# Optimization experiments

Measured on AMD Instinct MI355X. Metric: run time of the kernel, lower is better.

Reference implementation:

```python
import jax, jax.numpy as jnp
import numpy as np

TOP_K = 2


def setup_inputs() -> dict:
    key = jax.random.key(0)
    ks = jax.random.split(key, 5)
    B, S, D, F, E = 2, 1024, 2048, 4096, 8
    scale_in = 1.0 / np.sqrt(D)
    scale_f = 1.0 / np.sqrt(F)
    return {
        "hidden_states": jax.random.normal(ks[0], (B, S, D), dtype=jnp.float32),
        "gate_w": jax.random.normal(ks[1], (D, E), dtype=jnp.float32) * scale_in,
        "w1": jax.random.normal(ks[2], (E, D, F), dtype=jnp.float32) * scale_in,
        "w3": jax.random.normal(ks[3], (E, D, F), dtype=jnp.float32) * scale_in,
        "w2": jax.random.normal(ks[4], (E, F, D), dtype=jnp.float32) * scale_f,
    }


def reference(hidden_states, gate_w, w1, w3, w2):
    orig_shape = hidden_states.shape
    D = orig_shape[-1]
    x = hidden_states.reshape(-1, D)                      # [T, D]
    E = gate_w.shape[-1]

    # Router: replicated linear (no bias), logits in fp32.
    router_logits = (x @ gate_w).astype(jnp.float32)      # [T, E]
    probs = jax.nn.softmax(router_logits, axis=-1)        # [T, E]
    topk_vals, topk_idx = jax.lax.top_k(probs, TOP_K)     # [T, K]
    # renormalize=False: use raw softmax probs of the selected experts.
    # Scatter top-k weights back to a dense [T, E] combine matrix.
    onehot = jax.nn.one_hot(topk_idx, E, dtype=probs.dtype)        # [T, K, E]
    combine = jnp.einsum("tke,tk->te", onehot, topk_vals)          # [T, E]

    # Dense-over-experts SwiGLU (reference for the fused grouped-GEMM).
    gate = jax.nn.silu(jnp.einsum("td,edf->etf", x, w1))  # [E, T, F]
    up = jnp.einsum("td,edf->etf", x, w3)                 # [E, T, F]
    expert_out = jnp.einsum("etf,efd->etd", gate * up, w2)  # [E, T, D]

    # Combine (this is the TP all-reduce + weighted sum in vllm).
    y = jnp.einsum("te,etd->td", combine, expert_out)     # [T, D]
    return y.reshape(orig_shape)
```

## Files before the change

kernel.cpp:

```cpp
#include <hip/hip_runtime.h>

typedef short v8s __attribute__((ext_vector_type(8)));
typedef float v4f __attribute__((ext_vector_type(4)));

#define T_TOK 2048
#define DD 2048
#define FF 4096
#define EE 8
#define BM 128
#define BN 128
#define BK 64
#define MT_MAX 40
#define MAXROWS 5120

#define WS_COUNTS 0
#define WS_FILL   32
#define WS_ROWOFF 64
#define WS_TOPE   128
#define WS_TOPW   (WS_TOPE + T_TOK * 2 * 4)
#define WS_IDS    (WS_TOPW + T_TOK * 2 * 4)
#define WS_WTS    (WS_IDS + MAXROWS * 4)
#define WS_ZERO   (WS_WTS + MAXROWS * 4)
#define WS_H      73984ul

#define SWZ(r, kb) ((r) * 128 + ((kb) ^ ((((r) ^ ((r) >> 3)) & 7) << 4)))

static __device__ __forceinline__ short f2bf(float f) {
  return __builtin_bit_cast(short, static_cast<__bf16>(f));
}

__global__ __launch_bounds__(256) void router_k(
    const float* __restrict__ x, const float* __restrict__ gw,
    int* __restrict__ counts, int* __restrict__ tope, float* __restrict__ topw) {
  const int lane = threadIdx.x & 63;
  const int t = blockIdx.x * 4 + (threadIdx.x >> 6);
  if (t >= T_TOK) return;
  float acc[EE] = {0.f, 0.f, 0.f, 0.f, 0.f, 0.f, 0.f, 0.f};
  const float* xr = x + (size_t)t * DD;
  for (int i = 0; i < DD / 64; ++i) {
    int k = i * 64 + lane;
    float xv = xr[k];
    const v4f* g = (const v4f*)(gw + (size_t)k * EE);
    v4f g0 = g[0], g1 = g[1];
    acc[0] += xv * g0[0]; acc[1] += xv * g0[1]; acc[2] += xv * g0[2]; acc[3] += xv * g0[3];
    acc[4] += xv * g1[0]; acc[5] += xv * g1[1]; acc[6] += xv * g1[2]; acc[7] += xv * g1[3];
  }
  #pragma unroll
  for (int e = 0; e < EE; ++e) {
    #pragma unroll
    for (int off = 32; off > 0; off >>= 1) acc[e] += __shfl_xor(acc[e], off);
  }
  if (lane == 0) {
    float m = acc[0];
    #pragma unroll
    for (int e = 1; e < EE; ++e) m = fmaxf(m, acc[e]);
    float p[EE], s = 0.f;
    #pragma unroll
    for (int e = 0; e < EE; ++e) { p[e] = expf(acc[e] - m); s += p[e]; }
    float inv = 1.f / s;
    #pragma unroll
    for (int e = 0; e < EE; ++e) p[e] *= inv;
    int e1 = 0;
    #pragma unroll
    for (int e = 1; e < EE; ++e) if (p[e] > p[e1]) e1 = e;
    int e2 = (e1 == 0) ? 1 : 0;
    #pragma unroll
    for (int e = 0; e < EE; ++e) if (e != e1 && p[e] > p[e2]) e2 = e;
    tope[2 * t] = e1;  tope[2 * t + 1] = e2;
    topw[2 * t] = p[e1]; topw[2 * t + 1] = p[e2];
    atomicAdd(&counts[e1], 1);
    atomicAdd(&counts[e2], 1);
  }
}

__global__ void offsets_k(const int* __restrict__ counts, int* __restrict__ rowoff) {
  if (threadIdx.x == 0) {
    int off = 0;
    #pragma unroll
    for (int e = 0; e < EE; ++e) {
      rowoff[e] = off;
      off += ((counts[e] + BM - 1) / BM) * BM;
    }
  }
}

__global__ __launch_bounds__(256) void scatter_k(
    const int* __restrict__ tope, const float* __restrict__ topw,
    const int* __restrict__ rowoff, int* __restrict__ fill,
    int* __restrict__ ids, float* __restrict__ wts) {
  const int t = blockIdx.x * 256 + threadIdx.x;
  if (t >= T_TOK) return;
  #pragma unroll
  for (int j = 0; j < 2; ++j) {
    int e = tope[2 * t + j];
    int pos = rowoff[e] + atomicAdd(&fill[e], 1);
    ids[pos] = t;
    wts[pos] = topw[2 * t + j];
  }
}

__global__ __launch_bounds__(256, 2) void gemm1_k(
    const float* __restrict__ x, const float* __restrict__ w1,
    const float* __restrict__ w3, const int* __restrict__ counts,
    const int* __restrict__ rowoff, const int* __restrict__ ids,
    unsigned short* __restrict__ H) {
  const int nt = blockIdx.x, mt = blockIdx.y;
  int expert = -1;
  #pragma unroll
  for (int e = 0; e < EE; ++e) {
    int rs = rowoff[e];
    int tl = (counts[e] + BM - 1) / BM;
    if (mt * BM >= rs && mt * BM < rs + tl * BM) expert = e;
  }
  if (expert < 0) return;
  const int m0 = mt * BM, n0 = nt * BN;

  __shared__ unsigned short sA[BM * BK];
  __shared__ unsigned short sB0[BN * BK];
  __shared__ unsigned short sB1[BN * BK];

  const int tid = threadIdx.x;
  const int lane = tid & 63;
  const int wid = tid >> 6;
  const int wm = (wid >> 1) * 64, wn = (wid & 1) * 64;
  const int lr = lane & 15, lg = lane >> 4;

  const int a_row0 = tid >> 3;
  const int a_kc = (tid & 7) * 8;
  const float* aptr[4];
  #pragma unroll
  for (int g = 0; g < 4; ++g)
    aptr[g] = x + (size_t)ids[m0 + a_row0 + g * 32] * DD + a_kc;

  const int b_f4 = (tid & 31) * 4;
  const int b_k8 = (tid >> 5) * 8;
  const float* wb1 = w1 + (size_t)expert * DD * FF + n0 + b_f4 + (size_t)b_k8 * FF;
  const float* wb3 = w3 + (size_t)expert * DD * FF + n0 + b_f4 + (size_t)b_k8 * FF;

  v4f acc1[4][4], acc3[4][4];
  #pragma unroll
  for (int i = 0; i < 4; ++i)
    #pragma unroll
    for (int j = 0; j < 4; ++j) {
      acc1[i][j] = (v4f){0.f, 0.f, 0.f, 0.f};
      acc3[i][j] = (v4f){0.f, 0.f, 0.f, 0.f};
    }

  for (int kt = 0; kt < DD / BK; ++kt) {
    #pragma unroll
    for (int g = 0; g < 4; ++g) {
      const float* p = aptr[g] + (size_t)kt * BK;
      v4f u0 = *(const v4f*)p;
      v4f u1 = *(const v4f*)(p + 4);
      v8s h;
      h[0] = f2bf(u0[0]); h[1] = f2bf(u0[1]); h[2] = f2bf(u0[2]); h[3] = f2bf(u0[3]);
      h[4] = f2bf(u1[0]); h[5] = f2bf(u1[1]); h[6] = f2bf(u1[2]); h[7] = f2bf(u1[3]);
      *(v8s*)((char*)sA + SWZ(a_row0 + g * 32, a_kc * 2)) = h;
    }
    {
      const float* p = wb1 + (size_t)kt * BK * FF;
      v4f r[8];
      #pragma unroll
      for (int j = 0; j < 8; ++j) r[j] = *(const v4f*)(p + (size_t)j * FF);
      #pragma unroll
      for (int c = 0; c < 4; ++c) {
        v8s h;
        #pragma unroll
        for (int j = 0; j < 8; ++j) h[j] = f2bf(r[j][c]);
        *(v8s*)((char*)sB0 + SWZ(b_f4 + c, b_k8 * 2)) = h;
      }
      p = wb3 + (size_t)kt * BK * FF;
      #pragma unroll
      for (int j = 0; j < 8; ++j) r[j] = *(const v4f*)(p + (size_t)j * FF);
      #pragma unroll
      for (int c = 0; c < 4; ++c) {
        v8s h;
        #pragma unroll
        for (int j = 0; j < 8; ++j) h[j] = f2bf(r[j][c]);
        *(v8s*)((char*)sB1 + SWZ(b_f4 + c, b_k8 * 2)) = h;
      }
    }
    __syncthreads();
    #pragma unroll
    for (int ks = 0; ks < 2; ++ks) {
      const int kb = ks * 64 + lg * 16;
      v8s a[4], b1[4], b3[4];
      #pragma unroll
      for (int m = 0; m < 4; ++m)
        a[m] = *(const v8s*)((const char*)sA + SWZ(wm + m * 16 + lr, kb));
      #pragma unroll
      for (int n = 0; n < 4; ++n) {
        b1[n] = *(const v8s*)((const char*)sB0 + SWZ(wn + n * 16 + lr, kb));
        b3[n] = *(const v8s*)((const char*)sB1 + SWZ(wn + n * 16 + lr, kb));
      }
      #pragma unroll
      for (int m = 0; m < 4; ++m)
        #pragma unroll
        for (int n = 0; n < 4; ++n) {
          acc1[m][n] = __builtin_amdgcn_mfma_f32_16x16x32_bf16(a[m], b1[n], acc1[m][n], 0, 0, 0);
          acc3[m][n] = __builtin_amdgcn_mfma_f32_16x16x32_bf16(a[m], b3[n], acc3[m][n], 0, 0, 0);
        }
    }
    __syncthreads();
  }
  #pragma unroll
  for (int m = 0; m < 4; ++m)
    #pragma unroll
    for (int n = 0; n < 4; ++n)
      #pragma unroll
      for (int r = 0; r < 4; ++r) {
        int row = wm + m * 16 + lg * 4 + r;
        int col = wn + n * 16 + lr;
        float g = acc1[m][n][r];
        float u = acc3[m][n][r];
        float hv = (g / (1.f + expf(-g))) * u;
        H[(size_t)(m0 + row) * FF + (n0 + col)] = (unsigned short)f2bf(hv);
      }
}

__global__ __launch_bounds__(256, 2) void gemm2_k(
    const unsigned short* __restrict__ H, const float* __restrict__ w2,
    const int* __restrict__ counts, const int* __restrict__ rowoff,
    const int* __restrict__ ids, const float* __restrict__ wts,
    float* __restrict__ out) {
  const int nt = blockIdx.x, mt = blockIdx.y;
  int expert = -1;
  #pragma unroll
  for (int e = 0; e < EE; ++e) {
    int rs = rowoff[e];
    int tl = (counts[e] + BM - 1) / BM;
    if (mt * BM >= rs && mt * BM < rs + tl * BM) expert = e;
  }
  if (expert < 0) return;
  const int m0 = mt * BM, n0 = nt * BN;

  __shared__ unsigned short sA[BM * BK];
  __shared__ unsigned short sB[BN * BK];

  const int tid = threadIdx.x;
  const int lane = tid & 63;
  const int wid = tid >> 6;
  const int wm = (wid >> 1) * 64, wn = (wid & 1) * 64;
  const int lr = lane & 15, lg = lane >> 4;

  const int a_row0 = tid >> 3;
  const int a_kc = (tid & 7) * 8;
  const unsigned short* ha = H + (size_t)(m0 + a_row0) * FF + a_kc;
  const int b_f4 = (tid & 31) * 4;
  const int b_k8 = (tid >> 5) * 8;
  const float* wb = w2 + (size_t)expert * FF * DD + n0 + b_f4 + (size_t)b_k8 * DD;

  v4f acc[4][4];
  #pragma unroll
  for (int i = 0; i < 4; ++i)
    #pragma unroll
    for (int j = 0; j < 4; ++j) acc[i][j] = (v4f){0.f, 0.f, 0.f, 0.f};

  for (int kt = 0; kt < FF / BK; ++kt) {
    #pragma unroll
    for (int g = 0; g < 4; ++g) {
      v8s h = *(const v8s*)(ha + (size_t)g * 32 * FF + kt * BK);
      *(v8s*)((char*)sA + SWZ(a_row0 + g * 32, a_kc * 2)) = h;
    }
    {
      const float* p = wb + (size_t)kt * BK * DD;
      v4f r[8];
      #pragma unroll
      for (int j = 0; j < 8; ++j) r[j] = *(const v4f*)(p + (size_t)j * DD);
      #pragma unroll
      for (int c = 0; c < 4; ++c) {
        v8s h;
        #pragma unroll
        for (int j = 0; j < 8; ++j) h[j] = f2bf(r[j][c]);
        *(v8s*)((char*)sB + SWZ(b_f4 + c, b_k8 * 2)) = h;
      }
    }
    __syncthreads();
    #pragma unroll
    for (int ks = 0; ks < 2; ++ks) {
      const int kb = ks * 64 + lg * 16;
      v8s a[4], b[4];
      #pragma unroll
      for (int m = 0; m < 4; ++m)
        a[m] = *(const v8s*)((const char*)sA + SWZ(wm + m * 16 + lr, kb));
      #pragma unroll
      for (int n = 0; n < 4; ++n)
        b[n] = *(const v8s*)((const char*)sB + SWZ(wn + n * 16 + lr, kb));
      #pragma unroll
      for (int m = 0; m < 4; ++m)
        #pragma unroll
        for (int n = 0; n < 4; ++n)
          acc[m][n] = __builtin_amdgcn_mfma_f32_16x16x32_bf16(a[m], b[n], acc[m][n], 0, 0, 0);
    }
    __syncthreads();
  }
  #pragma unroll
  for (int m = 0; m < 4; ++m)
    #pragma unroll
    for (int r = 0; r < 4; ++r) {
      int row = m0 + wm + m * 16 + lg * 4 + r;
      float wgt = wts[row];
      if (wgt != 0.f) {
        float* orow = out + (size_t)ids[row] * DD + n0 + wn + lr;
        #pragma unroll
        for (int n = 0; n < 4; ++n)
          atomicAdd(orow + n * 16, wgt * acc[m][n][r]);
      }
    }
}

extern "C" void kernel_launch(void* const* d_in, const int* in_sizes, int n_in,
                              void* d_out, int out_size, void* d_ws, size_t ws_size,
                              hipStream_t stream) {
  const float* x  = (const float*)d_in[0];
  const float* gw = (const float*)d_in[1];
  const float* w1 = (const float*)d_in[2];
  const float* w3 = (const float*)d_in[3];
  const float* w2 = (const float*)d_in[4];
  float* out = (float*)d_out;
  char* ws = (char*)d_ws;

  int*   counts = (int*)(ws + WS_COUNTS);
  int*   fill   = (int*)(ws + WS_FILL);
  int*   rowoff = (int*)(ws + WS_ROWOFF);
  int*   tope   = (int*)(ws + WS_TOPE);
  float* topw   = (float*)(ws + WS_TOPW);
  int*   ids    = (int*)(ws + WS_IDS);
  float* wts    = (float*)(ws + WS_WTS);
  unsigned short* H = (unsigned short*)(ws + WS_H);

  hipMemsetAsync(ws, 0, WS_ZERO, stream);
  hipMemsetAsync(d_out, 0, (size_t)out_size * sizeof(float), stream);

  router_k<<<T_TOK / 4, 256, 0, stream>>>(x, gw, counts, tope, topw);
  offsets_k<<<1, 64, 0, stream>>>(counts, rowoff);
  scatter_k<<<T_TOK / 256, 256, 0, stream>>>(tope, topw, rowoff, fill, ids, wts);
  gemm1_k<<<dim3(FF / BN, MT_MAX), 256, 0, stream>>>(x, w1, w3, counts, rowoff, ids, H);
  gemm2_k<<<dim3(DD / BN, MT_MAX), 256, 0, stream>>>(H, w2, counts, rowoff, ids, wts, out);
}
```

Before: 550.3 us.

## Use 32x32 MFMA, pre-convert activations to bf16, and XCD-aware block remap

Switches both grouped GEMMs from 16x16x32 to 32x32x16 bf16 MFMA tiles, which cuts LDS fragment reads per MFMA. A new kernel converts x to bf16 once up front, so gemm1 loads bf16 rows directly instead of converting fp32 per tile. Block indices are remapped so consecutive blocks land on the same XCD, aiming at better L2 reuse of weights. The costs are an extra kernel launch, 8 MB of workspace, and a changed epilogue layout.

```diff
diff --git a/kernel.cpp b/kernel.cpp
--- a/kernel.cpp
+++ b/kernel.cpp
@@ -2,6 +2,7 @@
 
 typedef short v8s __attribute__((ext_vector_type(8)));
 typedef float v4f __attribute__((ext_vector_type(4)));
+typedef float v16f __attribute__((ext_vector_type(16)));
 
 #define T_TOK 2048
 #define DD 2048
@@ -21,12 +22,24 @@
 #define WS_IDS    (WS_TOPW + T_TOK * 2 * 4)
 #define WS_WTS    (WS_IDS + MAXROWS * 4)
 #define WS_ZERO   (WS_WTS + MAXROWS * 4)
-#define WS_H      73984ul
+#define WS_XB     73984ul
+#define WS_H      (WS_XB + 8388608ul)
 
 #define SWZ(r, kb) ((r) * 128 + ((kb) ^ ((((r) ^ ((r) >> 3)) & 7) << 4)))
 
 static __device__ __forceinline__ short f2bf(float f) {
   return __builtin_bit_cast(short, static_cast<__bf16>(f));
+}
+
+__global__ __launch_bounds__(256) void xbf_k(const float* __restrict__ x,
+                                             unsigned short* __restrict__ xb) {
+  const int i = (blockIdx.x * 256 + threadIdx.x) * 8;
+  v4f a = *(const v4f*)(x + i);
+  v4f b = *(const v4f*)(x + i + 4);
+  v8s h;
+  h[0] = f2bf(a[0]); h[1] = f2bf(a[1]); h[2] = f2bf(a[2]); h[3] = f2bf(a[3]);
+  h[4] = f2bf(b[0]); h[5] = f2bf(b[1]); h[6] = f2bf(b[2]); h[7] = f2bf(b[3]);
+  *(v8s*)(xb + i) = h;
 }
 
 __global__ __launch_bounds__(256) void router_k(
@@ -99,12 +112,8 @@
   }
 }
 
-__global__ __launch_bounds__(256, 2) void gemm1_k(
-    const float* __restrict__ x, const float* __restrict__ w1,
-    const float* __restrict__ w3, const int* __restrict__ counts,
-    const int* __restrict__ rowoff, const int* __restrict__ ids,
-    unsigned short* __restrict__ H) {
-  const int nt = blockIdx.x, mt = blockIdx.y;
+static __device__ __forceinline__ int find_expert(
+    const int* counts, const int* rowoff, int mt) {
   int expert = -1;
   #pragma unroll
   for (int e = 0; e < EE; ++e) {
@@ -112,6 +121,27 @@
     int tl = (counts[e] + BM - 1) / BM;
     if (mt * BM >= rs && mt * BM < rs + tl * BM) expert = e;
   }
+  return expert;
+}
+
+static __device__ __forceinline__ void xcd_map(int* nt, int* mt) {
+  int gx = gridDim.x, gy = gridDim.y;
+  int nwg = gx * gy;
+  int lin = blockIdx.y * gx + blockIdx.x;
+  int q = nwg >> 3;
+  int s = (lin & 7) * q + (lin >> 3);
+  *nt = s / gy;
+  *mt = s % gy;
+}
+
+__global__ __launch_bounds__(256, 2) void gemm1_k(
+    const unsigned short* __restrict__ xb, const float* __restrict__ w1,
+    const float* __restrict__ w3, const int* __restrict__ counts,
+    const int* __restrict__ rowoff, const int* __restrict__ ids,
+    unsigned short* __restrict__ H) {
+  int nt, mt;
+  xcd_map(&nt, &mt);
+  const int expert = find_expert(counts, rowoff, mt);
   if (expert < 0) return;
   const int m0 = mt * BM, n0 = nt * BN;
 
@@ -123,39 +153,35 @@
   const int lane = tid & 63;
   const int wid = tid >> 6;
   const int wm = (wid >> 1) * 64, wn = (wid & 1) * 64;
-  const int lr = lane & 15, lg = lane >> 4;
+  const int l32 = lane & 31;
+  const int khi = lane >> 5;
 
   const int a_row0 = tid >> 3;
-  const int a_kc = (tid & 7) * 8;
-  const float* aptr[4];
+  const int a_ch = tid & 7;
+  const unsigned short* aptr[4];
   #pragma unroll
   for (int g = 0; g < 4; ++g)
-    aptr[g] = x + (size_t)ids[m0 + a_row0 + g * 32] * DD + a_kc;
+    aptr[g] = xb + (size_t)ids[m0 + a_row0 + g * 32] * DD + a_ch * 8;
 
   const int b_f4 = (tid & 31) * 4;
   const int b_k8 = (tid >> 5) * 8;
   const float* wb1 = w1 + (size_t)expert * DD * FF + n0 + b_f4 + (size_t)b_k8 * FF;
   const float* wb3 = w3 + (size_t)expert * DD * FF + n0 + b_f4 + (size_t)b_k8 * FF;
 
-  v4f acc1[4][4], acc3[4][4];
-  #pragma unroll
-  for (int i = 0; i < 4; ++i)
-    #pragma unroll
-    for (int j = 0; j < 4; ++j) {
-      acc1[i][j] = (v4f){0.f, 0.f, 0.f, 0.f};
-      acc3[i][j] = (v4f){0.f, 0.f, 0.f, 0.f};
+  v16f acc1[2][2], acc3[2][2];
+  #pragma unroll
+  for (int i = 0; i < 2; ++i)
+    #pragma unroll
+    for (int j = 0; j < 2; ++j) {
+      acc1[i][j] = (v16f)(0.f);
+      acc3[i][j] = (v16f)(0.f);
     }
 
   for (int kt = 0; kt < DD / BK; ++kt) {
     #pragma unroll
     for (int g = 0; g < 4; ++g) {
-      const float* p = aptr[g] + (size_t)kt * BK;
-      v4f u0 = *(const v4f*)p;
-      v4f u1 = *(const v4f*)(p + 4);
-      v8s h;
-      h[0] = f2bf(u0[0]); h[1] = f2bf(u0[1]); h[2] = f2bf(u0[2]); h[3] = f2bf(u0[3]);
-      h[4] = f2bf(u1[0]); h[5] = f2bf(u1[1]); h[6] = f2bf(u1[2]); h[7] = f2bf(u1[3]);
-      *(v8s*)((char*)sA + SWZ(a_row0 + g * 32, a_kc * 2)) = h;
+      v8s h = *(const v8s*)(aptr[g] + (size_t)kt * BK);
+      *(v8s*)((char*)sA + SWZ(a_row0 + g * 32, a_ch * 16)) = h;
     }
     {
       const float* p = wb1 + (size_t)kt * BK * FF;
@@ -182,35 +208,35 @@
     }
     __syncthreads();
     #pragma unroll
-    for (int ks = 0; ks < 2; ++ks) {
-      const int kb = ks * 64 + lg * 16;
-      v8s a[4], b1[4], b3[4];
-      #pragma unroll
-      for (int m = 0; m < 4; ++m)
-        a[m] = *(const v8s*)((const char*)sA + SWZ(wm + m * 16 + lr, kb));
-      #pragma unroll
-      for (int n = 0; n < 4; ++n) {
-        b1[n] = *(const v8s*)((const char*)sB0 + SWZ(wn + n * 16 + lr, kb));
-        b3[n] = *(const v8s*)((const char*)sB1 + SWZ(wn + n * 16 + lr, kb));
-      }
-      #pragma unroll
-      for (int m = 0; m < 4; ++m)
-        #pragma unroll
-        for (int n = 0; n < 4; ++n) {
-          acc1[m][n] = __builtin_amdgcn_mfma_f32_16x16x32_bf16(a[m], b1[n], acc1[m][n], 0, 0, 0);
-          acc3[m][n] = __builtin_amdgcn_mfma_f32_16x16x32_bf16(a[m], b3[n], acc3[m][n], 0, 0, 0);
+    for (int ks = 0; ks < 4; ++ks) {
+      const int kb = (ks * 2 + khi) * 16;
+      v8s a[2], b1[2], b3[2];
+      #pragma unroll
+      for (int m = 0; m < 2; ++m)
+        a[m] = *(const v8s*)((const char*)sA + SWZ(wm + m * 32 + l32, kb));
+      #pragma unroll
+      for (int n = 0; n < 2; ++n) {
+        b1[n] = *(const v8s*)((const char*)sB0 + SWZ(wn + n * 32 + l32, kb));
+        b3[n] = *(const v8s*)((const char*)sB1 + SWZ(wn + n * 32 + l32, kb));
+      }
+      #pragma unroll
+      for (int m = 0; m < 2; ++m)
+        #pragma unroll
+        for (int n = 0; n < 2; ++n) {
+          acc1[m][n] = __builtin_amdgcn_mfma_f32_32x32x16_bf16(a[m], b1[n], acc1[m][n], 0, 0, 0);
+          acc3[m][n] = __builtin_amdgcn_mfma_f32_32x32x16_bf16(a[m], b3[n], acc3[m][n], 0, 0, 0);
         }
     }
     __syncthreads();
   }
   #pragma unroll
-  for (int m = 0; m < 4; ++m)
-    #pragma unroll
-    for (int n = 0; n < 4; ++n)
-      #pragma unroll
-      for (int r = 0; r < 4; ++r) {
-        int row = wm + m * 16 + lg * 4 + r;
-        int col = wn + n * 16 + lr;
+  for (int m = 0; m < 2; ++m)
+    #pragma unroll
+    for (int n = 0; n < 2; ++n)
+      #pragma unroll
+      for (int r = 0; r < 16; ++r) {
+        int row = wm + m * 32 + (r & 3) + 8 * (r >> 2) + 4 * khi;
+        int col = wn + n * 32 + l32;
         float g = acc1[m][n][r];
         float u = acc3[m][n][r];
         float hv = (g / (1.f + expf(-g))) * u;
@@ -223,14 +249,9 @@
     const int* __restrict__ counts, const int* __restrict__ rowoff,
     const int* __restrict__ ids, const float* __restrict__ wts,
     float* __restrict__ out) {
-  const int nt = blockIdx.x, mt = blockIdx.y;
-  int expert = -1;
-  #pragma unroll
-  for (int e = 0; e < EE; ++e) {
-    int rs = rowoff[e];
-    int tl = (counts[e] + BM - 1) / BM;
-    if (mt * BM >= rs && mt * BM < rs + tl * BM) expert = e;
-  }
+  int nt, mt;
+  xcd_map(&nt, &mt);
+  const int expert = find_expert(counts, rowoff, mt);
   if (expert < 0) return;
   const int m0 = mt * BM, n0 = nt * BN;
 
@@ -241,26 +262,27 @@
   const int lane = tid & 63;
   const int wid = tid >> 6;
   const int wm = (wid >> 1) * 64, wn = (wid & 1) * 64;
-  const int lr = lane & 15, lg = lane >> 4;
+  const int l32 = lane & 31;
+  const int khi = lane >> 5;
 
   const int a_row0 = tid >> 3;
-  const int a_kc = (tid & 7) * 8;
-  const unsigned short* ha = H + (size_t)(m0 + a_row0) * FF + a_kc;
+  const int a_ch = tid & 7;
+  const unsigned short* ha = H + (size_t)(m0 + a_row0) * FF + a_ch * 8;
   const int b_f4 = (tid & 31) * 4;
   const int b_k8 = (tid >> 5) * 8;
   const float* wb = w2 + (size_t)expert * FF * DD + n0 + b_f4 + (size_t)b_k8 * DD;
 
-  v4f acc[4][4];
-  #pragma unroll
-  for (int i = 0; i < 4; ++i)
-    #pragma unroll
-    for (int j = 0; j < 4; ++j) acc[i][j] = (v4f){0.f, 0.f, 0.f, 0.f};
+  v16f acc[2][2];
+  #pragma unroll
+  for (int i = 0; i < 2; ++i)
+    #pragma unroll
+    for (int j = 0; j < 2; ++j) acc[i][j] = (v16f)(0.f);
 
   for (int kt = 0; kt < FF / BK; ++kt) {
     #pragma unroll
     for (int g = 0; g < 4; ++g) {
       v8s h = *(const v8s*)(ha + (size_t)g * 32 * FF + kt * BK);
-      *(v8s*)((char*)sA + SWZ(a_row0 + g * 32, a_kc * 2)) = h;
+      *(v8s*)((char*)sA + SWZ(a_row0 + g * 32, a_ch * 16)) = h;
     }
     {
       const float* p = wb + (size_t)kt * BK * DD;
@@ -277,34 +299,34 @@
     }
     __syncthreads();
     #pragma unroll
-    for (int ks = 0; ks < 2; ++ks) {
-      const int kb = ks * 64 + lg * 16;
-      v8s a[4], b[4];
-      #pragma unroll
-      for (int m = 0; m < 4; ++m)
-        a[m] = *(const v8s*)((const char*)sA + SWZ(wm + m * 16 + lr, kb));
-      #pragma unroll
-      for (int n = 0; n < 4; ++n)
-        b[n] = *(const v8s*)((const char*)sB + SWZ(wn + n * 16 + lr, kb));
-      #pragma unroll
-      for (int m = 0; m < 4; ++m)
-        #pragma unroll
-        for (int n = 0; n < 4; ++n)
-          acc[m][n] = __builtin_amdgcn_mfma_f32_16x16x32_bf16(a[m], b[n], acc[m][n], 0, 0, 0);
+    for (int ks = 0; ks < 4; ++ks) {
+      const int kb = (ks * 2 + khi) * 16;
+      v8s a[2], b[2];
+      #pragma unroll
+      for (int m = 0; m < 2; ++m)
+        a[m] = *(const v8s*)((const char*)sA + SWZ(wm + m * 32 + l32, kb));
+      #pragma unroll
+      for (int n = 0; n < 2; ++n)
+        b[n] = *(const v8s*)((const char*)sB + SWZ(wn + n * 32 + l32, kb));
+      #pragma unroll
+      for (int m = 0; m < 2; ++m)
+        #pragma unroll
+        for (int n = 0; n < 2; ++n)
+          acc[m][n] = __builtin_amdgcn_mfma_f32_32x32x16_bf16(a[m], b[n], acc[m][n], 0, 0, 0);
     }
     __syncthreads();
   }
   #pragma unroll
-  for (int m = 0; m < 4; ++m)
-    #pragma unroll
-    for (int r = 0; r < 4; ++r) {
-      int row = m0 + wm + m * 16 + lg * 4 + r;
+  for (int m = 0; m < 2; ++m)
+    #pragma unroll
+    for (int r = 0; r < 16; ++r) {
+      int row = m0 + wm + m * 32 + (r & 3) + 8 * (r >> 2) + 4 * khi;
       float wgt = wts[row];
       if (wgt != 0.f) {
-        float* orow = out + (size_t)ids[row] * DD + n0 + wn + lr;
-        #pragma unroll
-        for (int n = 0; n < 4; ++n)
-          atomicAdd(orow + n * 16, wgt * acc[m][n][r]);
+        float* orow = out + (size_t)ids[row] * DD + n0 + wn + l32;
+        #pragma unroll
+        for (int n = 0; n < 2; ++n)
+          atomicAdd(orow + n * 32, wgt * acc[m][n][r]);
       }
     }
 }
@@ -327,14 +349,16 @@
   float* topw   = (float*)(ws + WS_TOPW);
   int*   ids    = (int*)(ws + WS_IDS);
   float* wts    = (float*)(ws + WS_WTS);
-  unsigned short* H = (unsigned short*)(ws + WS_H);
+  unsigned short* xb = (unsigned short*)(ws + WS_XB);
+  unsigned short* H  = (unsigned short*)(ws + WS_H);
 
   hipMemsetAsync(ws, 0, WS_ZERO, stream);
   hipMemsetAsync(d_out, 0, (size_t)out_size * sizeof(float), stream);
 
+  xbf_k<<<T_TOK * DD / (256 * 8), 256, 0, stream>>>(x, xb);
   router_k<<<T_TOK / 4, 256, 0, stream>>>(x, gw, counts, tope, topw);
   offsets_k<<<1, 64, 0, stream>>>(counts, rowoff);
   scatter_k<<<T_TOK / 256, 256, 0, stream>>>(tope, topw, rowoff, fill, ids, wts);
-  gemm1_k<<<dim3(FF / BN, MT_MAX), 256, 0, stream>>>(x, w1, w3, counts, rowoff, ids, H);
+  gemm1_k<<<dim3(FF / BN, MT_MAX), 256, 0, stream>>>(xb, w1, w3, counts, rowoff, ids, H);
   gemm2_k<<<dim3(DD / BN, MT_MAX), 256, 0, stream>>>(H, w2, counts, rowoff, ids, wts, out);
 }
```

New measurement: 545.0 us. No clear change (-1.0%).
